# Kernel optimization log

Hardware: AMD Instinct MI355X
Metric: run time of the kernel (lower is better)

The kernel has to match this reference:

```python
import jax, jax.numpy as jnp
import numpy as np

B, N, D, H = 4, 4096, 128, 8
DH = D // H
EPS = 1e-6


def _layernorm(x, g, b):
    mu = jnp.mean(x, axis=-1, keepdims=True)
    var = jnp.var(x, axis=-1, keepdims=True)
    return (x - mu) * jax.lax.rsqrt(var + EPS) * g + b


def setup_inputs() -> dict:
    key = jax.random.key(0)
    ks = jax.random.split(key, 12)
    p = lambda k, shape: (jax.random.normal(k, shape, jnp.float32) * 0.02)
    x = jax.random.normal(ks[0], (B, N, D), jnp.float32)
    # scale fx so the sigmoid of the N-length contraction is not fully saturated
    fx = jax.random.normal(ks[1], (B, N, D), jnp.float32) / N
    return {
        "x": x,
        "fx": fx,
        "ln1_g": jnp.ones((D,), jnp.float32),
        "ln1_b": jnp.zeros((D,), jnp.float32),
        "wq": p(ks[2], (D, D)),
        "wk": p(ks[3], (D, D)),
        "wv": p(ks[4], (D, D)),
        "wo": p(ks[5], (D, D)),
        "bo": jnp.zeros((D,), jnp.float32),
        "ln2_g": jnp.ones((D,), jnp.float32),
        "ln2_b": jnp.zeros((D,), jnp.float32),
        "w1": p(ks[6], (D, D)),
        "b1": jnp.zeros((D,), jnp.float32),
        "w2": p(ks[7], (D, D)),
        "b2": jnp.zeros((D,), jnp.float32),
    }


def reference(x, fx, ln1_g, ln1_b, wq, wk, wv, wo, bo, ln2_g, ln2_b, w1, b1, w2, b2):
    b, n, d = x.shape
    h, dh = H, d // H
    # --- pre-norm linear self-attention ---
    xn = _layernorm(x, ln1_g, ln1_b)
    def heads(w):  # [b,n,d] @ w^T -> [b,h,n,dh]
        return jnp.einsum('bnd,ed->bne', xn, w).reshape(b, n, h, dh).transpose(0, 2, 1, 3)
    q = jax.nn.softmax(heads(wq), axis=-1)   # softmax over feature dim
    k = jax.nn.softmax(heads(wk), axis=2)    # softmax over sequence dim
    v = heads(wv)
    ctx = jnp.einsum('bhnd,bhne->bhde', k, v)         # [b,h,dh,dh]
    attn = jnp.einsum('bhnd,bhde->bhne', q, ctx)       # [b,h,n,dh]
    attn = attn.transpose(0, 2, 1, 3).reshape(b, n, d)
    attn = jnp.einsum('bnd,ed->bne', attn, wo) + bo
    x = x + attn                                       # residual (dropout=identity)
    # --- pre-norm MLP ---
    y = _layernorm(x, ln2_g, ln2_b)
    y = jax.nn.gelu(jnp.einsum('bnd,ed->bne', y, w1) + b1, approximate=False)
    y = jnp.einsum('bnd,ed->bne', y, w2) + b2
    x = x + y
    # --- quadratic update: sigmoid((x x^T) fx), as written in the module ---
    gram = jnp.einsum('bnd,bmd->bnm', x, x)            # [b,n,n] materialized, faithful
    fx = jax.nn.sigmoid(jnp.einsum('bnm,bmd->bnd', gram, fx))
    return (x, fx)
```

## Files before the change

kernel.cpp:

```cpp
#include <hip/hip_runtime.h>
#include <math.h>

#define BB 4
#define NN 4096
#define DD 128
#define MM (BB*NN)

typedef __attribute__((ext_vector_type(8))) short short8;
typedef __attribute__((ext_vector_type(4))) float f32x4;

__device__ inline short f2bf(float f) {
    unsigned u = __float_as_uint(f);
    u = (u + 0x7FFFu + ((u >> 16) & 1u)) >> 16;
    return (short)u;
}
__device__ inline float bf2f(short s) {
    return __uint_as_float(((unsigned)(unsigned short)s) << 16);
}
__device__ inline short8 pack_bf8(float4 a, float4 b) {
    short8 o;
    o[0] = f2bf(a.x); o[1] = f2bf(a.y); o[2] = f2bf(a.z); o[3] = f2bf(a.w);
    o[4] = f2bf(b.x); o[5] = f2bf(b.y); o[6] = f2bf(b.z); o[7] = f2bf(b.w);
    return o;
}
__device__ inline int swzoff(int row, int col) {
    return ((row * 128 + col) * 2) ^ ((row & 7) << 4);
}

__global__ __launch_bounds__(256) void wprep(const float* __restrict__ w0, const float* __restrict__ w1,
                                             const float* __restrict__ w2, const float* __restrict__ w3,
                                             const float* __restrict__ w4, short* __restrict__ wf) {
    int m = blockIdx.x >> 3;
    int j = (blockIdx.x & 7) * 256 + threadIdx.x;
    const float* W = (m == 0) ? w0 : (m == 1) ? w1 : (m == 2) ? w2 : (m == 3) ? w3 : w4;
    int nt = j >> 8, ks = (j >> 6) & 3, l = j & 63, r = l & 15, g = l >> 4;
    const float* src = W + (size_t)(nt * 16 + r) * DD + 32 * ks + 8 * g;
    float4 a = *(const float4*)src;
    float4 b = *(const float4*)(src + 4);
    ((short8*)(wf + (size_t)m * 16384))[j] = pack_bf8(a, b);
}

__global__ __launch_bounds__(256) void lnctx(const float* __restrict__ x,
                                             const float* __restrict__ lng,
                                             const float* __restrict__ lnb,
                                             const short* __restrict__ wf,
                                             float* __restrict__ partC,
                                             float* __restrict__ pcs) {
    __shared__ float ekL[32][132];
    __shared__ float vL[32][132];
    int t = threadIdx.x;
    int block_row = blockIdx.x * 32;
    int w = t >> 6, l = t & 63, r = l & 15, g = l >> 4;
    int rh = w >> 1, nt0 = (w & 1) << 2;
    int row0 = block_row + rh * 16;

    const float* ap = x + (size_t)(row0 + r) * DD + 8 * g;
    float4 av0[4], av1[4];
    #pragma unroll
    for (int ks = 0; ks < 4; ks++) {
        av0[ks] = *(const float4*)(ap + 32 * ks);
        av1[ks] = *(const float4*)(ap + 32 * ks + 4);
    }
    float s = 0.f, ss = 0.f;
    #pragma unroll
    for (int ks = 0; ks < 4; ks++) {
        float4 a = av0[ks], b = av1[ks];
        s  += a.x + a.y + a.z + a.w + b.x + b.y + b.z + b.w;
        ss += a.x*a.x + a.y*a.y + a.z*a.z + a.w*a.w + b.x*b.x + b.y*b.y + b.z*b.z + b.w*b.w;
    }
    s  += __shfl_xor(s, 16);  s  += __shfl_xor(s, 32);
    ss += __shfl_xor(ss, 16); ss += __shfl_xor(ss, 32);
    float mu = s * (1.0f / DD);
    float var = ss * (1.0f / DD) - mu * mu;
    float rs = rsqrtf(var + 1e-6f);

    short8 af[4];
    #pragma unroll
    for (int ks = 0; ks < 4; ks++) {
        float4 g0 = *(const float4*)(lng + 32 * ks + 8 * g);
        float4 g1 = *(const float4*)(lng + 32 * ks + 8 * g + 4);
        float4 b0 = *(const float4*)(lnb + 32 * ks + 8 * g);
        float4 b1 = *(const float4*)(lnb + 32 * ks + 8 * g + 4);
        float4 n0, n1;
        n0.x = (av0[ks].x - mu) * rs * g0.x + b0.x;
        n0.y = (av0[ks].y - mu) * rs * g0.y + b0.y;
        n0.z = (av0[ks].z - mu) * rs * g0.z + b0.z;
        n0.w = (av0[ks].w - mu) * rs * g0.w + b0.w;
        n1.x = (av1[ks].x - mu) * rs * g1.x + b1.x;
        n1.y = (av1[ks].y - mu) * rs * g1.y + b1.y;
        n1.z = (av1[ks].z - mu) * rs * g1.z + b1.z;
        n1.w = (av1[ks].w - mu) * rs * g1.w + b1.w;
        af[ks] = pack_bf8(n0, n1);
    }

    f32x4 acc[2][4];
    #pragma unroll
    for (int m = 0; m < 2; m++)
        #pragma unroll
        for (int n = 0; n < 4; n++) acc[m][n] = (f32x4){0.f, 0.f, 0.f, 0.f};
    const short8* wp8 = (const short8*)wf;
    #pragma unroll
    for (int ks = 0; ks < 4; ks++)
        #pragma unroll
        for (int m = 0; m < 2; m++)
            #pragma unroll
            for (int n = 0; n < 4; n++)
                acc[m][n] = __builtin_amdgcn_mfma_f32_16x16x32_bf16(
                    af[ks], wp8[(size_t)m * 2048 + ((nt0 + n) * 4 + ks) * 64 + l], acc[m][n], 0, 0, 0);

    #pragma unroll
    for (int n = 0; n < 4; n++) {
        int col = (nt0 + n) * 16 + r;
        #pragma unroll
        for (int j = 0; j < 4; j++) {
            int rowL = rh * 16 + 4 * g + j;
            ekL[rowL][col] = __expf(acc[0][n][j]);
            vL[rowL][col]  = acc[1][n][j];
        }
    }
    __syncthreads();

    int h = t >> 5, sub = t & 31, d = sub >> 1, e0 = (sub & 1) * 8;
    float cs = 0.f;
    float sc[8] = {0.f, 0.f, 0.f, 0.f, 0.f, 0.f, 0.f, 0.f};
    #pragma unroll 8
    for (int row = 0; row < 32; row++) {
        float ekv = ekL[row][h * 16 + d];
        float4 v0 = *(const float4*)&vL[row][h * 16 + e0];
        float4 v1 = *(const float4*)&vL[row][h * 16 + e0 + 4];
        sc[0] += ekv * v0.x; sc[1] += ekv * v0.y; sc[2] += ekv * v0.z; sc[3] += ekv * v0.w;
        sc[4] += ekv * v1.x; sc[5] += ekv * v1.y; sc[6] += ekv * v1.z; sc[7] += ekv * v1.w;
        cs += ekv;
    }
    float* cb = partC + (size_t)blockIdx.x * 2048 + h * 256 + d * 16 + e0;
    *(float4*)cb       = (float4){sc[0], sc[1], sc[2], sc[3]};
    *(float4*)(cb + 4) = (float4){sc[4], sc[5], sc[6], sc[7]};
    if ((sub & 1) == 0) pcs[(size_t)blockIdx.x * 128 + h * 16 + d] = cs;
}

__global__ __launch_bounds__(256) void ctxred(const float* __restrict__ part,
                                              float* __restrict__ ctxacc) {
    int k = blockIdx.x;
    int b = k >> 4, s0 = (k & 15) * 128;
    int t = threadIdx.x;
    int slot = s0 + (t & 127), half = t >> 7;
    float s = 0.f;
    #pragma unroll 8
    for (int c = half * 64; c < half * 64 + 64; c++)
        s += part[(size_t)((b << 7) + c) * 2048 + slot];
    __shared__ float red[128];
    if (half) red[t & 127] = s;
    __syncthreads();
    if (!half) ctxacc[(size_t)b * 2048 + slot] = s + red[t & 127];
}

__global__ __launch_bounds__(256) void build_mt_k(const float* __restrict__ ctxacc,
                                                  const float* __restrict__ pcs,
                                                  const float* __restrict__ wo,
                                                  short* __restrict__ mtfrag) {
    int b = blockIdx.x >> 3, nt = blockIdx.x & 7;
    int t = threadIdx.x;
    __shared__ float ctxL[2048];
    __shared__ float csL[128];
    __shared__ float woL[2048];
    #pragma unroll
    for (int i = 0; i < 8; i++) {
        int idx = i * 256 + t;
        ctxL[idx] = ctxacc[(size_t)b * 2048 + idx];
        woL[idx]  = wo[(size_t)(nt * 16) * DD + idx];
    }
    if (t < 128) {
        float s = 0.f;
        #pragma unroll 8
        for (int c = 0; c < 128; c++) s += pcs[(size_t)(b * 128 + c) * 128 + t];
        csL[t] = s;
    }
    __syncthreads();
    int ks = (t >> 6) & 3, l = t & 63, r = l & 15, g = l >> 4;
    short8 o;
    #pragma unroll
    for (int i2 = 0; i2 < 8; i2++) {
        int k = 32 * ks + 8 * g + i2;
        float inv = 1.0f / csL[k];
        const float* wrow = woL + r * DD + (k >> 4) * 16;
        float s = 0.f;
        #pragma unroll
        for (int eo = 0; eo < 16; eo++) s += ctxL[k * 16 + eo] * wrow[eo];
        o[i2] = f2bf(s * inv);
    }
    ((short8*)(mtfrag + (size_t)b * 16384))[nt * 256 + t] = o;
}

__global__ __launch_bounds__(256) void fused_mid(const float* __restrict__ x,
                                                 const float* __restrict__ ln1g,
                                                 const float* __restrict__ ln1b,
                                                 const short* __restrict__ wqf,
                                                 const short* __restrict__ mtf,
                                                 const float* __restrict__ bo,
                                                 const float* __restrict__ ln2g,
                                                 const float* __restrict__ ln2b,
                                                 const short* __restrict__ w1f,
                                                 const float* __restrict__ b1,
                                                 const short* __restrict__ w2f,
                                                 const float* __restrict__ b2,
                                                 float* __restrict__ xfinal,
                                                 short* __restrict__ xbf) {
    __shared__ __align__(16) char ex[32 * 128 * 2];
    __shared__ float ex2f[32][132];
    __shared__ float redS[4][16], redSS[4][16];
    int t = threadIdx.x;
    int block_row = blockIdx.x * 32;
    int w = t >> 6, l = t & 63, r = l & 15, g = l >> 4;
    int rh = w >> 1, nt0 = (w & 1) << 2;
    int row0 = block_row + rh * 16;
    int rrow = rh * 16 + r;

    const float* ap = x + (size_t)(row0 + r) * DD + 8 * g;
    float4 av0[4], av1[4];
    #pragma unroll
    for (int ks = 0; ks < 4; ks++) {
        av0[ks] = *(const float4*)(ap + 32 * ks);
        av1[ks] = *(const float4*)(ap + 32 * ks + 4);
    }
    if ((w & 1) == 0) {
        #pragma unroll
        for (int ks = 0; ks < 4; ks++) {
            *(float4*)&ex2f[rrow][32 * ks + 8 * g]     = av0[ks];
            *(float4*)&ex2f[rrow][32 * ks + 8 * g + 4] = av1[ks];
        }
    }
    float s = 0.f, ss = 0.f;
    #pragma unroll
    for (int ks = 0; ks < 4; ks++) {
        float4 a = av0[ks], b = av1[ks];
        s  += a.x + a.y + a.z + a.w + b.x + b.y + b.z + b.w;
        ss += a.x*a.x + a.y*a.y + a.z*a.z + a.w*a.w + b.x*b.x + b.y*b.y + b.z*b.z + b.w*b.w;
    }
    s  += __shfl_xor(s, 16);  s  += __shfl_xor(s, 32);
    ss += __shfl_xor(ss, 16); ss += __shfl_xor(ss, 32);
    float mu1 = s * (1.0f / DD);
    float var1 = ss * (1.0f / DD) - mu1 * mu1;
    float rs1 = rsqrtf(var1 + 1e-6f);
    short8 af[4];
    #pragma unroll
    for (int ks = 0; ks < 4; ks++) {
        float4 g0 = *(const float4*)(ln1g + 32 * ks + 8 * g);
        float4 g1 = *(const float4*)(ln1g + 32 * ks + 8 * g + 4);
        float4 b0 = *(const float4*)(ln1b + 32 * ks + 8 * g);
        float4 b1v = *(const float4*)(ln1b + 32 * ks + 8 * g + 4);
        float4 n0, n1;
        n0.x = (av0[ks].x - mu1) * rs1 * g0.x + b0.x;
        n0.y = (av0[ks].y - mu1) * rs1 * g0.y + b0.y;
        n0.z = (av0[ks].z - mu1) * rs1 * g0.z + b0.z;
        n0.w = (av0[ks].w - mu1) * rs1 * g0.w + b0.w;
        n1.x = (av1[ks].x - mu1) * rs1 * g1.x + b1v.x;
        n1.y = (av1[ks].y - mu1) * rs1 * g1.y + b1v.y;
        n1.z = (av1[ks].z - mu1) * rs1 * g1.z + b1v.z;
        n1.w = (av1[ks].w - mu1) * rs1 * g1.w + b1v.w;
        af[ks] = pack_bf8(n0, n1);
    }

    const short8* qp = (const short8*)wqf;
    f32x4 accq[4];
    #pragma unroll
    for (int n = 0; n < 4; n++) accq[n] = (f32x4){0.f, 0.f, 0.f, 0.f};
    #pragma unroll
    for (int ks = 0; ks < 4; ks++)
        #pragma unroll
        for (int n = 0; n < 4; n++)
            accq[n] = __builtin_amdgcn_mfma_f32_16x16x32_bf16(
                af[ks], qp[((nt0 + n) * 4 + ks) * 64 + l], accq[n], 0, 0, 0);
    #pragma unroll
    for (int n = 0; n < 4; n++) {
        int col = (nt0 + n) * 16 + r;
        #pragma unroll
        for (int j = 0; j < 4; j++) {
            float e = __expf(accq[n][j]);
            float sm = e;
            sm += __shfl_xor(sm, 1); sm += __shfl_xor(sm, 2);
            sm += __shfl_xor(sm, 4); sm += __shfl_xor(sm, 8);
            *(short*)(ex + swzoff(rh * 16 + 4 * g + j, col)) = f2bf(e / sm);
        }
    }
    __syncthreads();

    short8 qf[4];
    #pragma unroll
    for (int ks = 0; ks < 4; ks++)
        qf[ks] = *(const short8*)(ex + swzoff(rrow, 32 * ks + 8 * g));
    float xres[4][4];
    #pragma unroll
    for (int n = 0; n < 4; n++)
        #pragma unroll
        for (int j = 0; j < 4; j++)
            xres[n][j] = ex2f[rh * 16 + 4 * g + j][(nt0 + n) * 16 + r];

    const short8* mp = (const short8*)(mtf + (size_t)(block_row >> 12) * 16384);
    f32x4 acc[4];
    #pragma unroll
    for (int n = 0; n < 4; n++) acc[n] = (f32x4){0.f, 0.f, 0.f, 0.f};
    #pragma unroll
    for (int ks = 0; ks < 4; ks++)
        #pragma unroll
        for (int n = 0; n < 4; n++)
            acc[n] = __builtin_amdgcn_mfma_f32_16x16x32_bf16(
                qf[ks], mp[((nt0 + n) * 4 + ks) * 64 + l], acc[n], 0, 0, 0);

    float vv[4][4];
    #pragma unroll
    for (int n = 0; n < 4; n++) {
        int col = (nt0 + n) * 16 + r;
        float bv = bo[col];
        #pragma unroll
        for (int j = 0; j < 4; j++)
            vv[n][j] = acc[n][j] + bv + xres[n][j];
    }

    #pragma unroll
    for (int j = 0; j < 4; j++) {
        float s1  = vv[0][j] + vv[1][j] + vv[2][j] + vv[3][j];
        float s2 = vv[0][j]*vv[0][j] + vv[1][j]*vv[1][j] + vv[2][j]*vv[2][j] + vv[3][j]*vv[3][j];
        s1 += __shfl_xor(s1, 1); s1 += __shfl_xor(s1, 2); s1 += __shfl_xor(s1, 4); s1 += __shfl_xor(s1, 8);
        s2 += __shfl_xor(s2, 1); s2 += __shfl_xor(s2, 2); s2 += __shfl_xor(s2, 4); s2 += __shfl_xor(s2, 8);
        if (r == 0) { redS[w][4 * g + j] = s1; redSS[w][4 * g + j] = s2; }
    }
    __syncthreads();
    int base = w & 2;
    #pragma unroll
    for (int j = 0; j < 4; j++) {
        int rr = 4 * g + j;
        float S  = redS[base][rr]  + redS[base + 1][rr];
        float SS = redSS[base][rr] + redSS[base + 1][rr];
        float mu = S * (1.0f / DD);
        float var = SS * (1.0f / DD) - mu * mu;
        float rs = rsqrtf(var + 1e-6f);
        int rowL = rh * 16 + rr;
        #pragma unroll
        for (int n = 0; n < 4; n++) {
            int col = (nt0 + n) * 16 + r;
            float y = (vv[n][j] - mu) * rs * ln2g[col] + ln2b[col];
            *(short*)(ex + swzoff(rowL, col)) = f2bf(y);
        }
    }
    __syncthreads();
    short8 yf[4];
    #pragma unroll
    for (int ks = 0; ks < 4; ks++)
        yf[ks] = *(const short8*)(ex + swzoff(rrow, 32 * ks + 8 * g));
    __syncthreads();
    const short8* w1p = (const short8*)w1f;
    f32x4 acc2[4];
    #pragma unroll
    for (int n = 0; n < 4; n++) acc2[n] = (f32x4){0.f, 0.f, 0.f, 0.f};
    #pragma unroll
    for (int ks = 0; ks < 4; ks++)
        #pragma unroll
        for (int n = 0; n < 4; n++)
            acc2[n] = __builtin_amdgcn_mfma_f32_16x16x32_bf16(
                yf[ks], w1p[((nt0 + n) * 4 + ks) * 64 + l], acc2[n], 0, 0, 0);
    #pragma unroll
    for (int n = 0; n < 4; n++) {
        int col = (nt0 + n) * 16 + r;
        float bv = b1[col];
        #pragma unroll
        for (int j = 0; j < 4; j++) {
            float v = acc2[n][j] + bv;
            v = 0.5f * v * (1.0f + erff(v * 0.70710678118654752f));
            *(short*)(ex + swzoff(rh * 16 + 4 * g + j, col)) = f2bf(v);
        }
    }
    __syncthreads();
    short8 hf[4];
    #pragma unroll
    for (int ks = 0; ks < 4; ks++)
        hf[ks] = *(const short8*)(ex + swzoff(rrow, 32 * ks + 8 * g));
    const short8* w2p = (const short8*)w2f;
    f32x4 acc3[4];
    #pragma unroll
    for (int n = 0; n < 4; n++) acc3[n] = (f32x4){0.f, 0.f, 0.f, 0.f};
    #pragma unroll
    for (int ks = 0; ks < 4; ks++)
        #pragma unroll
        for (int n = 0; n < 4; n++)
            acc3[n] = __builtin_amdgcn_mfma_f32_16x16x32_bf16(
                hf[ks], w2p[((nt0 + n) * 4 + ks) * 64 + l], acc3[n], 0, 0, 0);
    #pragma unroll
    for (int n = 0; n < 4; n++) {
        int col = (nt0 + n) * 16 + r;
        float bv = b2[col];
        #pragma unroll
        for (int j = 0; j < 4; j++) {
            float v = acc3[n][j] + bv + vv[n][j];
            size_t row = (size_t)(row0 + 4 * g + j);
            xfinal[row * DD + col] = v;
            xbf[row * DD + col] = f2bf(v);
        }
    }
}

__global__ __launch_bounds__(512) void sbuild_p(const short* __restrict__ xf,
                                                const float* __restrict__ fx,
                                                short* __restrict__ part) {
    int b = blockIdx.x >> 6, chunk = blockIdx.x & 63;
    int t = threadIdx.x;
    __shared__ float xs[64 * 128], fs[64 * 128];
    const short* xb = xf + ((size_t)b * NN + chunk * 64) * DD;
    const float* fb = fx + ((size_t)b * NN + chunk * 64) * DD;
    const short8* xg = (const short8*)xb;
    float4* xs4 = (float4*)xs; float4* fs4 = (float4*)fs;
    const float4* fg = (const float4*)fb;
    #pragma unroll
    for (int i = 0; i < 2; i++) {
        int j = i * 512 + t;
        short8 s8 = xg[j];
        float4 a = {bf2f(s8[0]), bf2f(s8[1]), bf2f(s8[2]), bf2f(s8[3])};
        float4 c = {bf2f(s8[4]), bf2f(s8[5]), bf2f(s8[6]), bf2f(s8[7])};
        xs4[2 * j] = a; xs4[2 * j + 1] = c;
    }
    #pragma unroll
    for (int i = 0; i < 4; i++) {
        int j = i * 512 + t;
        fs4[j] = fg[j];
    }
    __syncthreads();
    int td = t & 15, te = t >> 4;
    float acc[8][4];
    #pragma unroll
    for (int a = 0; a < 8; a++)
        #pragma unroll
        for (int c = 0; c < 4; c++) acc[a][c] = 0.f;
    for (int r = 0; r < 64; r++) {
        float4 x0 = xs4[r * 32 + td * 2], x1 = xs4[r * 32 + td * 2 + 1];
        float4 f0 = fs4[r * 32 + te];
        float xv[8] = {x0.x, x0.y, x0.z, x0.w, x1.x, x1.y, x1.z, x1.w};
        float fv[4] = {f0.x, f0.y, f0.z, f0.w};
        #pragma unroll
        for (int a = 0; a < 8; a++)
            #pragma unroll
            for (int c = 0; c < 4; c++) acc[a][c] = fmaf(xv[a], fv[c], acc[a][c]);
    }
    short* pb = part + (size_t)blockIdx.x * 16384;
    #pragma unroll
    for (int ci = 0; ci < 4; ci++) {
        short8 o;
        #pragma unroll
        for (int a = 0; a < 8; a++) o[a] = f2bf(acc[a][ci]);
        *(short8*)(pb + (size_t)(te * 4 + ci) * 128 + td * 8) = o;
    }
}

__global__ __launch_bounds__(256) void sreduce2(const short* __restrict__ part,
                                                float* __restrict__ S_T) {
    int b = blockIdx.x >> 7, e = blockIdx.x & 127;
    int t = threadIdx.x;
    int d8 = (t & 15) * 8;
    int ch0 = t >> 4;
    float s[8] = {0.f, 0.f, 0.f, 0.f, 0.f, 0.f, 0.f, 0.f};
    #pragma unroll
    for (int cc = 0; cc < 4; cc++) {
        int ch = ch0 + cc * 16;
        short8 u = *(const short8*)(part + (size_t)(b * 64 + ch) * 16384 + e * 128 + d8);
        #pragma unroll
        for (int i = 0; i < 8; i++) s[i] += bf2f(u[i]);
    }
    #pragma unroll
    for (int i = 0; i < 8; i++) {
        s[i] += __shfl_xor(s[i], 16);
        s[i] += __shfl_xor(s[i], 32);
    }
    __shared__ float red[4][128];
    int w = t >> 6;
    if ((t & 63) < 16) {
        #pragma unroll
        for (int i = 0; i < 8; i++) red[w][d8 + i] = s[i];
    }
    __syncthreads();
    if (t < 128)
        S_T[((size_t)b * 128 + e) * 128 + t] = red[0][t] + red[1][t] + red[2][t] + red[3][t];
}

__global__ __launch_bounds__(256) void gemm_sig(const short* __restrict__ A,
                                                const float* __restrict__ S_T,
                                                float* __restrict__ Cf) {
    int t = threadIdx.x;
    int block_row = blockIdx.x * 32;
    int w = t >> 6, l = t & 63, r = l & 15, g = l >> 4;
    int row0 = block_row + ((w >> 1) << 4);
    int nt0 = (w & 1) << 2;
    const short8* ap = (const short8*)(A + (size_t)(row0 + r) * DD + 8 * g);
    short8 af[4];
    #pragma unroll
    for (int ks = 0; ks < 4; ks++) af[ks] = ap[ks * 4];
    const float* sp = S_T + (size_t)(block_row >> 12) * 16384;
    short8 bf[4][4];
// ... 23 lines not shown
        for (int j = 0; j < 4; j++) {
            float v = 1.0f / (1.0f + __expf(-acc[n][j]));
            Cf[(size_t)(row0 + 4 * g + j) * DD + col] = v;
        }
    }
}

extern "C" void kernel_launch(void* const* d_in, const int* in_sizes, int n_in,
                              void* d_out, int out_size, void* d_ws, size_t ws_size,
                              hipStream_t stream) {
    const float* x    = (const float*)d_in[0];
    const float* fx   = (const float*)d_in[1];
    const float* ln1g = (const float*)d_in[2];
    const float* ln1b = (const float*)d_in[3];
    const float* wq   = (const float*)d_in[4];
    const float* wk   = (const float*)d_in[5];
    const float* wv   = (const float*)d_in[6];
    const float* wo   = (const float*)d_in[7];
    const float* bo   = (const float*)d_in[8];
    const float* ln2g = (const float*)d_in[9];
    const float* ln2b = (const float*)d_in[10];
    const float* w1   = (const float*)d_in[11];
    const float* b1   = (const float*)d_in[12];
    const float* w2   = (const float*)d_in[13];
    const float* b2   = (const float*)d_in[14];

    float* out = (float*)d_out;
    float* xfinal = out;
    float* fxout  = out + (size_t)MM * DD;

    float* ws = (float*)d_ws;
    short* xbf    = (short*)ws;
    short* partSb = (short*)(ws + 1048576);
    short* wfW    = (short*)(ws + 3145728);
    float* partC  = ws + 3145728 + 40960;
    float* pcs    = partC + 1048576;
    float* ctxacc = pcs + 65536;
    float* S_T    = ctxacc + 8192;
    short* mtf    = (short*)(S_T + 65536);

    wprep<<<40, 256, 0, stream>>>(wq, wk, wv, w1, w2, wfW);
    lnctx<<<512, 256, 0, stream>>>(x, ln1g, ln1b, wfW + 16384, partC, pcs);
    ctxred<<<64, 256, 0, stream>>>(partC, ctxacc);
    build_mt_k<<<32, 256, 0, stream>>>(ctxacc, pcs, wo, mtf);
    fused_mid<<<512, 256, 0, stream>>>(x, ln1g, ln1b, wfW, mtf, bo, ln2g, ln2b,
                                       wfW + 3 * 16384, b1, wfW + 4 * 16384, b2,
                                       xfinal, xbf);
    sbuild_p<<<256, 512, 0, stream>>>(xbf, fx, partSb);
    sreduce2<<<512, 256, 0, stream>>>(partSb, S_T);
    gemm_sig<<<512, 256, 0, stream>>>(xbf, S_T, fxout);
}
```

Measured before the change: 73.06 us.

## Fuse x^T·fx partial-sum build into the mid MLP kernel

The separate sbuild_p kernel is removed. Its per-chunk x^T·fx partial products are now computed at the end of fused_mid from the fp32 x values already in registers, staged through a shared-memory arena. This drops one launch and the re-read of xbf and fx in a separate pass, and uses fp32 x instead of a bf16 round-trip. In exchange there are twice as many partial chunks (128 per batch of 32 rows), which doubles the partial-buffer writes and the sreduce2 reads. Shared-memory use per block also grows.

Measured after the change: 78.42 us. 1.07x slower.

```diff
diff --git a/kernel.cpp b/kernel.cpp
--- a/kernel.cpp
+++ b/kernel.cpp
@@ -191,23 +191,27 @@
     ((short8*)(mtfrag + (size_t)b * 16384))[nt * 256 + t] = o;
 }
 
-__global__ __launch_bounds__(256) void fused_mid(const float* __restrict__ x,
-                                                 const float* __restrict__ ln1g,
-                                                 const float* __restrict__ ln1b,
-                                                 const short* __restrict__ wqf,
-                                                 const short* __restrict__ mtf,
-                                                 const float* __restrict__ bo,
-                                                 const float* __restrict__ ln2g,
-                                                 const float* __restrict__ ln2b,
-                                                 const short* __restrict__ w1f,
-                                                 const float* __restrict__ b1,
-                                                 const short* __restrict__ w2f,
-                                                 const float* __restrict__ b2,
-                                                 float* __restrict__ xfinal,
-                                                 short* __restrict__ xbf) {
-    __shared__ __align__(16) char ex[32 * 128 * 2];
-    __shared__ float ex2f[32][132];
-    __shared__ float redS[4][16], redSS[4][16];
+__global__ __launch_bounds__(256) void fused_mid_s(const float* __restrict__ x,
+                                                   const float* __restrict__ fx,
+                                                   const float* __restrict__ ln1g,
+                                                   const float* __restrict__ ln1b,
+                                                   const short* __restrict__ wqf,
+                                                   const short* __restrict__ mtf,
+                                                   const float* __restrict__ bo,
+                                                   const float* __restrict__ ln2g,
+                                                   const float* __restrict__ ln2b,
+                                                   const short* __restrict__ w1f,
+                                                   const float* __restrict__ b1,
+                                                   const short* __restrict__ w2f,
+                                                   const float* __restrict__ b2,
+                                                   float* __restrict__ xfinal,
+                                                   short* __restrict__ xbf,
+                                                   short* __restrict__ partSb) {
+    __shared__ __align__(16) char arena[33792];
+    char* ex = arena;
+    float (*ex2f)[132] = (float(*)[132])(arena + 8192);
+    float (*redS)[16]  = (float(*)[16])(arena + 25088);
+    float (*redSS)[16] = (float(*)[16])(arena + 25344);
     int t = threadIdx.x;
     int block_row = blockIdx.x * 32;
     int w = t >> 6, l = t & 63, r = l & 15, g = l >> 4;
@@ -318,7 +322,7 @@
 
     #pragma unroll
     for (int j = 0; j < 4; j++) {
-        float s1  = vv[0][j] + vv[1][j] + vv[2][j] + vv[3][j];
+        float s1 = vv[0][j] + vv[1][j] + vv[2][j] + vv[3][j];
         float s2 = vv[0][j]*vv[0][j] + vv[1][j]*vv[1][j] + vv[2][j]*vv[2][j] + vv[3][j]*vv[3][j];
         s1 += __shfl_xor(s1, 1); s1 += __shfl_xor(s1, 2); s1 += __shfl_xor(s1, 4); s1 += __shfl_xor(s1, 8);
         s2 += __shfl_xor(s2, 1); s2 += __shfl_xor(s2, 2); s2 += __shfl_xor(s2, 4); s2 += __shfl_xor(s2, 8);
@@ -384,6 +388,7 @@
         for (int n = 0; n < 4; n++)
             acc3[n] = __builtin_amdgcn_mfma_f32_16x16x32_bf16(
                 hf[ks], w2p[((nt0 + n) * 4 + ks) * 64 + l], acc3[n], 0, 0, 0);
+    float xf_[4][4];
     #pragma unroll
     for (int n = 0; n < 4; n++) {
         int col = (nt0 + n) * 16 + r;
@@ -391,61 +396,58 @@
         #pragma unroll
         for (int j = 0; j < 4; j++) {
             float v = acc3[n][j] + bv + vv[n][j];
+            xf_[n][j] = v;
             size_t row = (size_t)(row0 + 4 * g + j);
             xfinal[row * DD + col] = v;
             xbf[row * DD + col] = f2bf(v);
         }
     }
-}
-
-__global__ __launch_bounds__(512) void sbuild_p(const short* __restrict__ xf,
-                                                const float* __restrict__ fx,
-                                                short* __restrict__ part) {
-    int b = blockIdx.x >> 6, chunk = blockIdx.x & 63;
-    int t = threadIdx.x;
-    __shared__ float xs[64 * 128], fs[64 * 128];
-    const short* xb = xf + ((size_t)b * NN + chunk * 64) * DD;
-    const float* fb = fx + ((size_t)b * NN + chunk * 64) * DD;
-    const short8* xg = (const short8*)xb;
-    float4* xs4 = (float4*)xs; float4* fs4 = (float4*)fs;
-    const float4* fg = (const float4*)fb;
-    #pragma unroll
-    for (int i = 0; i < 2; i++) {
-        int j = i * 512 + t;
-        short8 s8 = xg[j];
-        float4 a = {bf2f(s8[0]), bf2f(s8[1]), bf2f(s8[2]), bf2f(s8[3])};
-        float4 c = {bf2f(s8[4]), bf2f(s8[5]), bf2f(s8[6]), bf2f(s8[7])};
-        xs4[2 * j] = a; xs4[2 * j + 1] = c;
-    }
-    #pragma unroll
-    for (int i = 0; i < 4; i++) {
-        int j = i * 512 + t;
-        fs4[j] = fg[j];
-    }
-    __syncthreads();
-    int td = t & 15, te = t >> 4;
-    float acc[8][4];
-    #pragma unroll
-    for (int a = 0; a < 8; a++)
-        #pragma unroll
-        for (int c = 0; c < 4; c++) acc[a][c] = 0.f;
-    for (int r = 0; r < 64; r++) {
-        float4 x0 = xs4[r * 32 + td * 2], x1 = xs4[r * 32 + td * 2 + 1];
-        float4 f0 = fs4[r * 32 + te];
-        float xv[8] = {x0.x, x0.y, x0.z, x0.w, x1.x, x1.y, x1.z, x1.w};
-        float fv[4] = {f0.x, f0.y, f0.z, f0.w};
+
+    __syncthreads();
+    float* xsf = (float*)arena;
+    float* fsf = (float*)(arena + 16384);
+    {
+        const float4* fg = (const float4*)(fx + (size_t)block_row * DD);
+        float4* fsf4 = (float4*)fsf;
+        #pragma unroll
+        for (int i = 0; i < 4; i++) fsf4[i * 256 + t] = fg[i * 256 + t];
+        #pragma unroll
+        for (int n = 0; n < 4; n++) {
+            int col = (nt0 + n) * 16 + r;
+            #pragma unroll
+            for (int j = 0; j < 4; j++)
+                xsf[(rh * 16 + 4 * g + j) * 128 + col] = xf_[n][j];
+        }
+    }
+    __syncthreads();
+    {
+        int td = t >> 4, te = t & 15;
+        float accS[8][8];
         #pragma unroll
         for (int a = 0; a < 8; a++)
             #pragma unroll
-            for (int c = 0; c < 4; c++) acc[a][c] = fmaf(xv[a], fv[c], acc[a][c]);
-    }
-    short* pb = part + (size_t)blockIdx.x * 16384;
-    #pragma unroll
-    for (int ci = 0; ci < 4; ci++) {
-        short8 o;
-        #pragma unroll
-        for (int a = 0; a < 8; a++) o[a] = f2bf(acc[a][ci]);
-        *(short8*)(pb + (size_t)(te * 4 + ci) * 128 + td * 8) = o;
+            for (int c = 0; c < 8; c++) accS[a][c] = 0.f;
+        const float4* xs4 = (const float4*)xsf;
+        const float4* fs4 = (const float4*)fsf;
+        for (int row = 0; row < 32; row++) {
+            float4 x0 = xs4[row * 32 + td * 2], x1 = xs4[row * 32 + td * 2 + 1];
+            float4 f0 = fs4[row * 32 + te * 2], f1 = fs4[row * 32 + te * 2 + 1];
+            float xv[8] = {x0.x, x0.y, x0.z, x0.w, x1.x, x1.y, x1.z, x1.w};
+            float fv[8] = {f0.x, f0.y, f0.z, f0.w, f1.x, f1.y, f1.z, f1.w};
+            #pragma unroll
+            for (int a = 0; a < 8; a++)
+                #pragma unroll
+                for (int c = 0; c < 8; c++) accS[a][c] = fmaf(xv[a], fv[c], accS[a][c]);
+        }
+        short* pb = partSb + (size_t)blockIdx.x * 16384;
+        int d0 = td * 8, e0 = te * 8;
+        #pragma unroll
+        for (int ei = 0; ei < 8; ei++) {
+            short8 o;
+            #pragma unroll
+            for (int i = 0; i < 8; i++) o[i] = f2bf(accS[i][ei]);
+            *(short8*)(pb + (size_t)(e0 + ei) * DD + d0) = o;
+        }
     }
 }
 
@@ -457,9 +459,9 @@
     int ch0 = t >> 4;
     float s[8] = {0.f, 0.f, 0.f, 0.f, 0.f, 0.f, 0.f, 0.f};
     #pragma unroll
-    for (int cc = 0; cc < 4; cc++) {
+    for (int cc = 0; cc < 8; cc++) {
         int ch = ch0 + cc * 16;
-        short8 u = *(const short8*)(part + (size_t)(b * 64 + ch) * 16384 + e * 128 + d8);
+        short8 u = *(const short8*)(part + (size_t)(b * 128 + ch) * 16384 + e * 128 + d8);
         #pragma unroll
         for (int i = 0; i < 8; i++) s[i] += bf2f(u[i]);
     }
@@ -549,8 +551,8 @@
     float* ws = (float*)d_ws;
     short* xbf    = (short*)ws;
     short* partSb = (short*)(ws + 1048576);
-    short* wfW    = (short*)(ws + 3145728);
-    float* partC  = ws + 3145728 + 40960;
+    short* wfW    = (short*)(ws + 5242880);
+    float* partC  = ws + 5242880 + 40960;
     float* pcs    = partC + 1048576;
     float* ctxacc = pcs + 65536;
     float* S_T    = ctxacc + 8192;
@@ -560,10 +562,9 @@
     lnctx<<<512, 256, 0, stream>>>(x, ln1g, ln1b, wfW + 16384, partC, pcs);
     ctxred<<<64, 256, 0, stream>>>(partC, ctxacc);
     build_mt_k<<<32, 256, 0, stream>>>(ctxacc, pcs, wo, mtf);
-    fused_mid<<<512, 256, 0, stream>>>(x, ln1g, ln1b, wfW, mtf, bo, ln2g, ln2b,
-                                       wfW + 3 * 16384, b1, wfW + 4 * 16384, b2,
-                                       xfinal, xbf);
-    sbuild_p<<<256, 512, 0, stream>>>(xbf, fx, partSb);
+    fused_mid_s<<<512, 256, 0, stream>>>(x, fx, ln1g, ln1b, wfW, mtf, bo, ln2g, ln2b,
+                                         wfW + 3 * 16384, b1, wfW + 4 * 16384, b2,
+                                         xfinal, xbf, partSb);
     sreduce2<<<512, 256, 0, stream>>>(partSb, S_T);
     gemm_sig<<<512, 256, 0, stream>>>(xbf, S_T, fxout);
 }
```

## Split K dimension across wave pairs in fused_mid with LDS partial-sum reduction

Applied to the files above, without the earlier changes.

Doubles fused_mid's block to 512 threads, so each wave handles half of the K=128 contraction for every MFMA GEMM. The upper-half waves write their partial accumulators to LDS and the lower-half waves add them before the softmax, LayerNorm, GELU and output epilogues. The goal is more waves per block to hide latency, given only 512 blocks. In exchange it adds several extra __syncthreads and LDS round-trips per stage, and half the waves sit idle during the epilogues.

Measured after the change: 73.40 us. About the same (+0.5%).

```diff
diff --git a/kernel.cpp b/kernel.cpp
--- a/kernel.cpp
+++ b/kernel.cpp
@@ -191,7 +191,7 @@
     ((short8*)(mtfrag + (size_t)b * 16384))[nt * 256 + t] = o;
 }
 
-__global__ __launch_bounds__(256) void fused_mid(const float* __restrict__ x,
+__global__ __launch_bounds__(512) void fused_mid(const float* __restrict__ x,
                                                  const float* __restrict__ ln1g,
                                                  const float* __restrict__ ln1b,
                                                  const short* __restrict__ wqf,
@@ -205,59 +205,69 @@
                                                  const float* __restrict__ b2,
                                                  float* __restrict__ xfinal,
                                                  short* __restrict__ xbf) {
-    __shared__ __align__(16) char ex[32 * 128 * 2];
+    __shared__ __align__(16) char ex[8192];
     __shared__ float ex2f[32][132];
-    __shared__ float redS[4][16], redSS[4][16];
+    __shared__ f32x4 cbuf[16][64];
+    __shared__ float redA[8][16], redB[8][16];
+    __shared__ float redS[8][16], redSS[8][16];
     int t = threadIdx.x;
+    int w = t >> 6, l = t & 63, r = l & 15, g = l >> 4;
+    int rh = w >> 2, kh = (w >> 1) & 1, ch = w & 1;
+    int nt0 = ch * 4;
     int block_row = blockIdx.x * 32;
-    int w = t >> 6, l = t & 63, r = l & 15, g = l >> 4;
-    int rh = w >> 1, nt0 = (w & 1) << 2;
     int row0 = block_row + rh * 16;
     int rrow = rh * 16 + r;
-
-    const float* ap = x + (size_t)(row0 + r) * DD + 8 * g;
-    float4 av0[4], av1[4];
-    #pragma unroll
-    for (int ks = 0; ks < 4; ks++) {
-        av0[ks] = *(const float4*)(ap + 32 * ks);
-        av1[ks] = *(const float4*)(ap + 32 * ks + 4);
-    }
-    if ((w & 1) == 0) {
-        #pragma unroll
-        for (int ks = 0; ks < 4; ks++) {
-            *(float4*)&ex2f[rrow][32 * ks + 8 * g]     = av0[ks];
-            *(float4*)&ex2f[rrow][32 * ks + 8 * g + 4] = av1[ks];
+    int kbase = kh * 64;
+    int cslot = (rh * 2 + ch) * 4;
+
+    const float* ap = x + (size_t)(row0 + r) * DD + kbase + 8 * g;
+    float4 av0[2], av1[2];
+    #pragma unroll
+    for (int k2 = 0; k2 < 2; k2++) {
+        av0[k2] = *(const float4*)(ap + 32 * k2);
+        av1[k2] = *(const float4*)(ap + 32 * k2 + 4);
+    }
+    if (ch == 0) {
+        #pragma unroll
+        for (int k2 = 0; k2 < 2; k2++) {
+            *(float4*)&ex2f[rrow][kbase + 32 * k2 + 8 * g]     = av0[k2];
+            *(float4*)&ex2f[rrow][kbase + 32 * k2 + 8 * g + 4] = av1[k2];
         }
     }
     float s = 0.f, ss = 0.f;
     #pragma unroll
-    for (int ks = 0; ks < 4; ks++) {
-        float4 a = av0[ks], b = av1[ks];
+    for (int k2 = 0; k2 < 2; k2++) {
+        float4 a = av0[k2], b = av1[k2];
         s  += a.x + a.y + a.z + a.w + b.x + b.y + b.z + b.w;
         ss += a.x*a.x + a.y*a.y + a.z*a.z + a.w*a.w + b.x*b.x + b.y*b.y + b.z*b.z + b.w*b.w;
     }
     s  += __shfl_xor(s, 16);  s  += __shfl_xor(s, 32);
     ss += __shfl_xor(ss, 16); ss += __shfl_xor(ss, 32);
-    float mu1 = s * (1.0f / DD);
-    float var1 = ss * (1.0f / DD) - mu1 * mu1;
+    if (l < 16) { redA[w][l] = s; redB[w][l] = ss; }
+    __syncthreads();
+    float S1 = redA[rh * 4 + ch][r] + redA[rh * 4 + 2 + ch][r];
+    float S2 = redB[rh * 4 + ch][r] + redB[rh * 4 + 2 + ch][r];
+    float mu1 = S1 * (1.0f / DD);
+    float var1 = S2 * (1.0f / DD) - mu1 * mu1;
     float rs1 = rsqrtf(var1 + 1e-6f);
-    short8 af[4];
-    #pragma unroll
-    for (int ks = 0; ks < 4; ks++) {
-        float4 g0 = *(const float4*)(ln1g + 32 * ks + 8 * g);
-        float4 g1 = *(const float4*)(ln1g + 32 * ks + 8 * g + 4);
-        float4 b0 = *(const float4*)(ln1b + 32 * ks + 8 * g);
-        float4 b1v = *(const float4*)(ln1b + 32 * ks + 8 * g + 4);
+    short8 af[2];
+    #pragma unroll
+    for (int k2 = 0; k2 < 2; k2++) {
+        int co = kbase + 32 * k2 + 8 * g;
+        float4 g0 = *(const float4*)(ln1g + co);
+        float4 g1 = *(const float4*)(ln1g + co + 4);
+        float4 b0 = *(const float4*)(ln1b + co);
+        float4 b1v = *(const float4*)(ln1b + co + 4);
         float4 n0, n1;
-        n0.x = (av0[ks].x - mu1) * rs1 * g0.x + b0.x;
-        n0.y = (av0[ks].y - mu1) * rs1 * g0.y + b0.y;
-        n0.z = (av0[ks].z - mu1) * rs1 * g0.z + b0.z;
-        n0.w = (av0[ks].w - mu1) * rs1 * g0.w + b0.w;
-        n1.x = (av1[ks].x - mu1) * rs1 * g1.x + b1v.x;
-        n1.y = (av1[ks].y - mu1) * rs1 * g1.y + b1v.y;
-        n1.z = (av1[ks].z - mu1) * rs1 * g1.z + b1v.z;
-        n1.w = (av1[ks].w - mu1) * rs1 * g1.w + b1v.w;
-        af[ks] = pack_bf8(n0, n1);
+        n0.x = (av0[k2].x - mu1) * rs1 * g0.x + b0.x;
+        n0.y = (av0[k2].y - mu1) * rs1 * g0.y + b0.y;
+        n0.z = (av0[k2].z - mu1) * rs1 * g0.z + b0.z;
+        n0.w = (av0[k2].w - mu1) * rs1 * g0.w + b0.w;
+        n1.x = (av1[k2].x - mu1) * rs1 * g1.x + b1v.x;
+        n1.y = (av1[k2].y - mu1) * rs1 * g1.y + b1v.y;
+        n1.z = (av1[k2].z - mu1) * rs1 * g1.z + b1v.z;
+        n1.w = (av1[k2].w - mu1) * rs1 * g1.w + b1v.w;
+        af[k2] = pack_bf8(n0, n1);
     }
 
     const short8* qp = (const short8*)wqf;
@@ -265,135 +275,163 @@
     #pragma unroll
     for (int n = 0; n < 4; n++) accq[n] = (f32x4){0.f, 0.f, 0.f, 0.f};
     #pragma unroll
-    for (int ks = 0; ks < 4; ks++)
+    for (int k2 = 0; k2 < 2; k2++)
         #pragma unroll
         for (int n = 0; n < 4; n++)
             accq[n] = __builtin_amdgcn_mfma_f32_16x16x32_bf16(
-                af[ks], qp[((nt0 + n) * 4 + ks) * 64 + l], accq[n], 0, 0, 0);
-    #pragma unroll
-    for (int n = 0; n < 4; n++) {
-        int col = (nt0 + n) * 16 + r;
-        #pragma unroll
-        for (int j = 0; j < 4; j++) {
-            float e = __expf(accq[n][j]);
-            float sm = e;
-            sm += __shfl_xor(sm, 1); sm += __shfl_xor(sm, 2);
-            sm += __shfl_xor(sm, 4); sm += __shfl_xor(sm, 8);
-            *(short*)(ex + swzoff(rh * 16 + 4 * g + j, col)) = f2bf(e / sm);
-        }
-    }
-    __syncthreads();
-
-    short8 qf[4];
-    #pragma unroll
-    for (int ks = 0; ks < 4; ks++)
-        qf[ks] = *(const short8*)(ex + swzoff(rrow, 32 * ks + 8 * g));
-    float xres[4][4];
-    #pragma unroll
-    for (int n = 0; n < 4; n++)
-        #pragma unroll
-        for (int j = 0; j < 4; j++)
-            xres[n][j] = ex2f[rh * 16 + 4 * g + j][(nt0 + n) * 16 + r];
+                af[k2], qp[((nt0 + n) * 4 + kh * 2 + k2) * 64 + l], accq[n], 0, 0, 0);
+    if (kh == 1) {
+        #pragma unroll
+        for (int n = 0; n < 4; n++) cbuf[cslot + n][l] = accq[n];
+    }
+    __syncthreads();
+    if (kh == 0) {
+        #pragma unroll
+        for (int n = 0; n < 4; n++) {
+            accq[n] += cbuf[cslot + n][l];
+            int col = (nt0 + n) * 16 + r;
+            #pragma unroll
+            for (int j = 0; j < 4; j++) {
+                float e = __expf(accq[n][j]);
+                float sm = e;
+                sm += __shfl_xor(sm, 1); sm += __shfl_xor(sm, 2);
+                sm += __shfl_xor(sm, 4); sm += __shfl_xor(sm, 8);
+                *(short*)(ex + swzoff(rh * 16 + 4 * g + j, col)) = f2bf(e / sm);
+            }
+        }
+    }
+    __syncthreads();
+
+    short8 qf[2];
+    #pragma unroll
+    for (int k2 = 0; k2 < 2; k2++)
+        qf[k2] = *(const short8*)(ex + swzoff(rrow, kbase + 32 * k2 + 8 * g));
 
     const short8* mp = (const short8*)(mtf + (size_t)(block_row >> 12) * 16384);
     f32x4 acc[4];
     #pragma unroll
     for (int n = 0; n < 4; n++) acc[n] = (f32x4){0.f, 0.f, 0.f, 0.f};
     #pragma unroll
-    for (int ks = 0; ks < 4; ks++)
+    for (int k2 = 0; k2 < 2; k2++)
         #pragma unroll
         for (int n = 0; n < 4; n++)
             acc[n] = __builtin_amdgcn_mfma_f32_16x16x32_bf16(
-                qf[ks], mp[((nt0 + n) * 4 + ks) * 64 + l], acc[n], 0, 0, 0);
+                qf[k2], mp[((nt0 + n) * 4 + kh * 2 + k2) * 64 + l], acc[n], 0, 0, 0);
+    if (kh == 1) {
+        #pragma unroll
+        for (int n = 0; n < 4; n++) cbuf[cslot + n][l] = acc[n];
+    }
+    __syncthreads();
 
     float vv[4][4];
-    #pragma unroll
-    for (int n = 0; n < 4; n++) {
-        int col = (nt0 + n) * 16 + r;
-        float bv = bo[col];
-        #pragma unroll
-        for (int j = 0; j < 4; j++)
-            vv[n][j] = acc[n][j] + bv + xres[n][j];
-    }
-
-    #pragma unroll
-    for (int j = 0; j < 4; j++) {
-        float s1  = vv[0][j] + vv[1][j] + vv[2][j] + vv[3][j];
-        float s2 = vv[0][j]*vv[0][j] + vv[1][j]*vv[1][j] + vv[2][j]*vv[2][j] + vv[3][j]*vv[3][j];
-        s1 += __shfl_xor(s1, 1); s1 += __shfl_xor(s1, 2); s1 += __shfl_xor(s1, 4); s1 += __shfl_xor(s1, 8);
-        s2 += __shfl_xor(s2, 1); s2 += __shfl_xor(s2, 2); s2 += __shfl_xor(s2, 4); s2 += __shfl_xor(s2, 8);
-        if (r == 0) { redS[w][4 * g + j] = s1; redSS[w][4 * g + j] = s2; }
-    }
-    __syncthreads();
-    int base = w & 2;
-    #pragma unroll
-    for (int j = 0; j < 4; j++) {
-        int rr = 4 * g + j;
-        float S  = redS[base][rr]  + redS[base + 1][rr];
-        float SS = redSS[base][rr] + redSS[base + 1][rr];
-        float mu = S * (1.0f / DD);
-        float var = SS * (1.0f / DD) - mu * mu;
-        float rs = rsqrtf(var + 1e-6f);
-        int rowL = rh * 16 + rr;
+    if (kh == 0) {
         #pragma unroll
         for (int n = 0; n < 4; n++) {
+            acc[n] += cbuf[cslot + n][l];
             int col = (nt0 + n) * 16 + r;
-            float y = (vv[n][j] - mu) * rs * ln2g[col] + ln2b[col];
-            *(short*)(ex + swzoff(rowL, col)) = f2bf(y);
-        }
-    }
-    __syncthreads();
-    short8 yf[4];
-    #pragma unroll
-    for (int ks = 0; ks < 4; ks++)
-        yf[ks] = *(const short8*)(ex + swzoff(rrow, 32 * ks + 8 * g));
-    __syncthreads();
+            float bv = bo[col];
+            #pragma unroll
+            for (int j = 0; j < 4; j++)
+                vv[n][j] = acc[n][j] + bv + ex2f[rh * 16 + 4 * g + j][col];
+        }
+        #pragma unroll
+        for (int j = 0; j < 4; j++) {
+            float s1 = vv[0][j] + vv[1][j] + vv[2][j] + vv[3][j];
+            float s2 = vv[0][j]*vv[0][j] + vv[1][j]*vv[1][j] + vv[2][j]*vv[2][j] + vv[3][j]*vv[3][j];
+            s1 += __shfl_xor(s1, 1); s1 += __shfl_xor(s1, 2); s1 += __shfl_xor(s1, 4); s1 += __shfl_xor(s1, 8);
+            s2 += __shfl_xor(s2, 1); s2 += __shfl_xor(s2, 2); s2 += __shfl_xor(s2, 4); s2 += __shfl_xor(s2, 8);
+            if (r == 0) { redS[w][4 * g + j] = s1; redSS[w][4 * g + j] = s2; }
+        }
+    }
+    __syncthreads();
+    if (kh == 0) {
+        #pragma unroll
+        for (int j = 0; j < 4; j++) {
+            int rr = 4 * g + j;
+            float Sv  = redS[rh * 4 + 0][rr] + redS[rh * 4 + 1][rr];
+            float SSv = redSS[rh * 4 + 0][rr] + redSS[rh * 4 + 1][rr];
+            float mu = Sv * (1.0f / DD);
+            float var = SSv * (1.0f / DD) - mu * mu;
+            float rs = rsqrtf(var + 1e-6f);
+            #pragma unroll
+            for (int n = 0; n < 4; n++) {
+                int col = (nt0 + n) * 16 + r;
+                float y = (vv[n][j] - mu) * rs * ln2g[col] + ln2b[col];
+                *(short*)(ex + swzoff(rh * 16 + rr, col)) = f2bf(y);
+            }
+        }
+    }
+    __syncthreads();
+
+    short8 yf[2];
+    #pragma unroll
+    for (int k2 = 0; k2 < 2; k2++)
+        yf[k2] = *(const short8*)(ex + swzoff(rrow, kbase + 32 * k2 + 8 * g));
+
     const short8* w1p = (const short8*)w1f;
     f32x4 acc2[4];
     #pragma unroll
     for (int n = 0; n < 4; n++) acc2[n] = (f32x4){0.f, 0.f, 0.f, 0.f};
     #pragma unroll
-    for (int ks = 0; ks < 4; ks++)
+    for (int k2 = 0; k2 < 2; k2++)
         #pragma unroll
         for (int n = 0; n < 4; n++)
             acc2[n] = __builtin_amdgcn_mfma_f32_16x16x32_bf16(
-                yf[ks], w1p[((nt0 + n) * 4 + ks) * 64 + l], acc2[n], 0, 0, 0);
-    #pragma unroll
-    for (int n = 0; n < 4; n++) {
-        int col = (nt0 + n) * 16 + r;
-        float bv = b1[col];
-        #pragma unroll
-        for (int j = 0; j < 4; j++) {
-            float v = acc2[n][j] + bv;
-            v = 0.5f * v * (1.0f + erff(v * 0.70710678118654752f));
-            *(short*)(ex + swzoff(rh * 16 + 4 * g + j, col)) = f2bf(v);
-        }
-    }
-    __syncthreads();
-    short8 hf[4];
-    #pragma unroll
-    for (int ks = 0; ks < 4; ks++)
-        hf[ks] = *(const short8*)(ex + swzoff(rrow, 32 * ks + 8 * g));
+                yf[k2], w1p[((nt0 + n) * 4 + kh * 2 + k2) * 64 + l], acc2[n], 0, 0, 0);
+    if (kh == 1) {
+        #pragma unroll
+        for (int n = 0; n < 4; n++) cbuf[cslot + n][l] = acc2[n];
+    }
+    __syncthreads();
+    if (kh == 0) {
+        #pragma unroll
+        for (int n = 0; n < 4; n++) {
+            acc2[n] += cbuf[cslot + n][l];
+            int col = (nt0 + n) * 16 + r;
+            float bv = b1[col];
+            #pragma unroll
+            for (int j = 0; j < 4; j++) {
+                float v = acc2[n][j] + bv;
+                v = 0.5f * v * (1.0f + erff(v * 0.70710678118654752f));
+                *(short*)(ex + swzoff(rh * 16 + 4 * g + j, col)) = f2bf(v);
+            }
+        }
+    }
+    __syncthreads();
+
+    short8 hf[2];
+    #pragma unroll
+    for (int k2 = 0; k2 < 2; k2++)
+        hf[k2] = *(const short8*)(ex + swzoff(rrow, kbase + 32 * k2 + 8 * g));
+
     const short8* w2p = (const short8*)w2f;
     f32x4 acc3[4];
     #pragma unroll
     for (int n = 0; n < 4; n++) acc3[n] = (f32x4){0.f, 0.f, 0.f, 0.f};
     #pragma unroll
-    for (int ks = 0; ks < 4; ks++)
+    for (int k2 = 0; k2 < 2; k2++)
         #pragma unroll
         for (int n = 0; n < 4; n++)
             acc3[n] = __builtin_amdgcn_mfma_f32_16x16x32_bf16(
-                hf[ks], w2p[((nt0 + n) * 4 + ks) * 64 + l], acc3[n], 0, 0, 0);
-    #pragma unroll
-    for (int n = 0; n < 4; n++) {
-        int col = (nt0 + n) * 16 + r;
-        float bv = b2[col];
-        #pragma unroll
-        for (int j = 0; j < 4; j++) {
-            float v = acc3[n][j] + bv + vv[n][j];
-            size_t row = (size_t)(row0 + 4 * g + j);
-            xfinal[row * DD + col] = v;
-            xbf[row * DD + col] = f2bf(v);
+                hf[k2], w2p[((nt0 + n) * 4 + kh * 2 + k2) * 64 + l], acc3[n], 0, 0, 0);
+    if (kh == 1) {
+        #pragma unroll
+        for (int n = 0; n < 4; n++) cbuf[cslot + n][l] = acc3[n];
+    }
+    __syncthreads();
+    if (kh == 0) {
+        #pragma unroll
+        for (int n = 0; n < 4; n++) {
+            acc3[n] += cbuf[cslot + n][l];
+            int col = (nt0 + n) * 16 + r;
+            float bv = b2[col];
+            #pragma unroll
+            for (int j = 0; j < 4; j++) {
+                float v = acc3[n][j] + bv + vv[n][j];
+                size_t row = (size_t)(row0 + 4 * g + j);
+                xfinal[row * DD + col] = v;
+                xbf[row * DD + col] = f2bf(v);
+            }
         }
     }
 }
@@ -560,7 +598,7 @@
     lnctx<<<512, 256, 0, stream>>>(x, ln1g, ln1b, wfW + 16384, partC, pcs);
     ctxred<<<64, 256, 0, stream>>>(partC, ctxacc);
     build_mt_k<<<32, 256, 0, stream>>>(ctxacc, pcs, wo, mtf);
-    fused_mid<<<512, 256, 0, stream>>>(x, ln1g, ln1b, wfW, mtf, bo, ln2g, ln2b,
+    fused_mid<<<512, 512, 0, stream>>>(x, ln1g, ln1b, wfW, mtf, bo, ln2g, ln2b,
                                        wfW + 3 * 16384, b1, wfW + 4 * 16384, b2,
                                        xfinal, xbf);
     sbuild_p<<<256, 512, 0, stream>>>(xbf, fx, partSb);
```

## Fuse weight prep into context kernel, drop ctx reduction kernel, use tanh GELU

Applied to the files above, without the earlier changes.

Merges the weight-to-bf16 prep into the first attention-context kernel and doubles its rows per block (512 threads, 64 rows), halving the partial-context count. The separate context-reduction launch is removed and build_mt_k now sums the partials itself. K/V weights are converted inline from fp32 global memory rather than read from the prepped buffer. The erf GELU is replaced with a tanh-style sigmoid approximation, which changes numerics slightly, and build_mt_k's serial 64-partial reduction over only 32 blocks may become a new bottleneck.

New measurement: 80.22 us. +9.8%, slower.

```diff
diff --git a/kernel.cpp b/kernel.cpp
--- a/kernel.cpp
+++ b/kernel.cpp
@@ -26,33 +26,42 @@
 __device__ inline int swzoff(int row, int col) {
     return ((row * 128 + col) * 2) ^ ((row & 7) << 4);
 }
-
-__global__ __launch_bounds__(256) void wprep(const float* __restrict__ w0, const float* __restrict__ w1,
-                                             const float* __restrict__ w2, const float* __restrict__ w3,
-                                             const float* __restrict__ w4, short* __restrict__ wf) {
-    int m = blockIdx.x >> 3;
-    int j = (blockIdx.x & 7) * 256 + threadIdx.x;
-    const float* W = (m == 0) ? w0 : (m == 1) ? w1 : (m == 2) ? w2 : (m == 3) ? w3 : w4;
-    int nt = j >> 8, ks = (j >> 6) & 3, l = j & 63, r = l & 15, g = l >> 4;
-    const float* src = W + (size_t)(nt * 16 + r) * DD + 32 * ks + 8 * g;
-    float4 a = *(const float4*)src;
-    float4 b = *(const float4*)(src + 4);
-    ((short8*)(wf + (size_t)m * 16384))[j] = pack_bf8(a, b);
-}
-
-__global__ __launch_bounds__(256) void lnctx(const float* __restrict__ x,
-                                             const float* __restrict__ lng,
-                                             const float* __restrict__ lnb,
-                                             const short* __restrict__ wf,
-                                             float* __restrict__ partC,
-                                             float* __restrict__ pcs) {
-    __shared__ float ekL[32][132];
-    __shared__ float vL[32][132];
+__device__ inline float gelu_f(float v) {
+    float z = 1.5957691f * (v + 0.044715f * v * v * v);
+    return v / (1.0f + __expf(-z));
+}
+
+__global__ __launch_bounds__(512) void lnctx2(const float* __restrict__ x,
+                                              const float* __restrict__ lng,
+                                              const float* __restrict__ lnb,
+                                              const float* __restrict__ wq,
+                                              const float* __restrict__ wk,
+                                              const float* __restrict__ wv,
+                                              const float* __restrict__ w1,
+                                              const float* __restrict__ w2,
+                                              short* __restrict__ wfW,
+                                              float* __restrict__ partC,
+                                              float* __restrict__ pcs) {
+    __shared__ float ekL[64][132];
+    __shared__ float vL[64][132];
     int t = threadIdx.x;
-    int block_row = blockIdx.x * 32;
+    int bid = blockIdx.x;
+
+    if (bid < 40 && t < 256) {
+        int m = bid >> 3;
+        int j = (bid & 7) * 256 + t;
+        const float* W = (m == 0) ? wq : (m == 1) ? wk : (m == 2) ? wv : (m == 3) ? w1 : w2;
+        int nt = j >> 8, ks = (j >> 6) & 3, ll = j & 63, rr = ll & 15, gg = ll >> 4;
+        const float* src = W + (size_t)(nt * 16 + rr) * DD + 32 * ks + 8 * gg;
+        ((short8*)(wfW + (size_t)m * 16384))[j] = pack_bf8(*(const float4*)src, *(const float4*)(src + 4));
+    }
+
     int w = t >> 6, l = t & 63, r = l & 15, g = l >> 4;
-    int rh = w >> 1, nt0 = (w & 1) << 2;
-    int row0 = block_row + rh * 16;
+    int grp = w >> 2, wi = w & 3;
+    int rh = wi >> 1, nt0 = (wi & 1) << 2;
+    int block_row = bid * 64;
+    int row0 = block_row + grp * 32 + rh * 16;
+    int rowL0 = grp * 32 + rh * 16;
 
     const float* ap = x + (size_t)(row0 + r) * DD + 8 * g;
     float4 av0[4], av1[4];
@@ -98,63 +107,46 @@
     for (int m = 0; m < 2; m++)
         #pragma unroll
         for (int n = 0; n < 4; n++) acc[m][n] = (f32x4){0.f, 0.f, 0.f, 0.f};
-    const short8* wp8 = (const short8*)wf;
-    #pragma unroll
-    for (int ks = 0; ks < 4; ks++)
-        #pragma unroll
-        for (int m = 0; m < 2; m++)
+    #pragma unroll
+    for (int ks = 0; ks < 4; ks++)
+        #pragma unroll
+        for (int m = 0; m < 2; m++) {
+            const float* Wm = m ? wv : wk;
             #pragma unroll
-            for (int n = 0; n < 4; n++)
-                acc[m][n] = __builtin_amdgcn_mfma_f32_16x16x32_bf16(
-                    af[ks], wp8[(size_t)m * 2048 + ((nt0 + n) * 4 + ks) * 64 + l], acc[m][n], 0, 0, 0);
+            for (int n = 0; n < 4; n++) {
+                const float* wsrc = Wm + (size_t)((nt0 + n) * 16 + r) * DD + 32 * ks + 8 * g;
+                short8 bfr = pack_bf8(*(const float4*)wsrc, *(const float4*)(wsrc + 4));
+                acc[m][n] = __builtin_amdgcn_mfma_f32_16x16x32_bf16(af[ks], bfr, acc[m][n], 0, 0, 0);
+            }
+        }
 
     #pragma unroll
     for (int n = 0; n < 4; n++) {
         int col = (nt0 + n) * 16 + r;
         #pragma unroll
         for (int j = 0; j < 4; j++) {
-            int rowL = rh * 16 + 4 * g + j;
+            int rowL = rowL0 + 4 * g + j;
             ekL[rowL][col] = __expf(acc[0][n][j]);
             vL[rowL][col]  = acc[1][n][j];
         }
     }
     __syncthreads();
 
-    int h = t >> 5, sub = t & 31, d = sub >> 1, e0 = (sub & 1) * 8;
+    int h = w, d = l >> 2, e0 = (l & 3) * 4;
     float cs = 0.f;
-    float sc[8] = {0.f, 0.f, 0.f, 0.f, 0.f, 0.f, 0.f, 0.f};
+    float sc[4] = {0.f, 0.f, 0.f, 0.f};
     #pragma unroll 8
-    for (int row = 0; row < 32; row++) {
+    for (int row = 0; row < 64; row++) {
         float ekv = ekL[row][h * 16 + d];
         float4 v0 = *(const float4*)&vL[row][h * 16 + e0];
-        float4 v1 = *(const float4*)&vL[row][h * 16 + e0 + 4];
         sc[0] += ekv * v0.x; sc[1] += ekv * v0.y; sc[2] += ekv * v0.z; sc[3] += ekv * v0.w;
-        sc[4] += ekv * v1.x; sc[5] += ekv * v1.y; sc[6] += ekv * v1.z; sc[7] += ekv * v1.w;
         cs += ekv;
     }
-    float* cb = partC + (size_t)blockIdx.x * 2048 + h * 256 + d * 16 + e0;
-    *(float4*)cb       = (float4){sc[0], sc[1], sc[2], sc[3]};
-    *(float4*)(cb + 4) = (float4){sc[4], sc[5], sc[6], sc[7]};
-    if ((sub & 1) == 0) pcs[(size_t)blockIdx.x * 128 + h * 16 + d] = cs;
-}
-
-__global__ __launch_bounds__(256) void ctxred(const float* __restrict__ part,
-                                              float* __restrict__ ctxacc) {
-    int k = blockIdx.x;
-    int b = k >> 4, s0 = (k & 15) * 128;
-    int t = threadIdx.x;
-    int slot = s0 + (t & 127), half = t >> 7;
-    float s = 0.f;
-    #pragma unroll 8
-    for (int c = half * 64; c < half * 64 + 64; c++)
-        s += part[(size_t)((b << 7) + c) * 2048 + slot];
-    __shared__ float red[128];
-    if (half) red[t & 127] = s;
-    __syncthreads();
-    if (!half) ctxacc[(size_t)b * 2048 + slot] = s + red[t & 127];
-}
-
-__global__ __launch_bounds__(256) void build_mt_k(const float* __restrict__ ctxacc,
+    *(float4*)(partC + (size_t)bid * 2048 + h * 256 + d * 16 + e0) = (float4){sc[0], sc[1], sc[2], sc[3]};
+    if ((l & 3) == 0) pcs[(size_t)bid * 128 + h * 16 + d] = cs;
+}
+
+__global__ __launch_bounds__(256) void build_mt_k(const float* __restrict__ partC,
                                                   const float* __restrict__ pcs,
                                                   const float* __restrict__ wo,
                                                   short* __restrict__ mtfrag) {
@@ -163,16 +155,25 @@
     __shared__ float ctxL[2048];
     __shared__ float csL[128];
     __shared__ float woL[2048];
+    {
+        float s[8] = {0.f,0.f,0.f,0.f,0.f,0.f,0.f,0.f};
+        for (int c = 0; c < 64; c++) {
+            const float* pp = partC + (size_t)(b * 64 + c) * 2048 + t;
+            #pragma unroll
+            for (int i = 0; i < 8; i++) s[i] += pp[i * 256];
+        }
+        #pragma unroll
+        for (int i = 0; i < 8; i++) ctxL[i * 256 + t] = s[i];
+    }
     #pragma unroll
     for (int i = 0; i < 8; i++) {
         int idx = i * 256 + t;
-        ctxL[idx] = ctxacc[(size_t)b * 2048 + idx];
-        woL[idx]  = wo[(size_t)(nt * 16) * DD + idx];
+        woL[idx] = wo[(size_t)(nt * 16) * DD + idx];
     }
     if (t < 128) {
         float s = 0.f;
         #pragma unroll 8
-        for (int c = 0; c < 128; c++) s += pcs[(size_t)(b * 128 + c) * 128 + t];
+        for (int c = 0; c < 64; c++) s += pcs[(size_t)(b * 64 + c) * 128 + t];
         csL[t] = s;
     }
     __syncthreads();
@@ -318,7 +319,7 @@
 
     #pragma unroll
     for (int j = 0; j < 4; j++) {
-        float s1  = vv[0][j] + vv[1][j] + vv[2][j] + vv[3][j];
+        float s1 = vv[0][j] + vv[1][j] + vv[2][j] + vv[3][j];
         float s2 = vv[0][j]*vv[0][j] + vv[1][j]*vv[1][j] + vv[2][j]*vv[2][j] + vv[3][j]*vv[3][j];
         s1 += __shfl_xor(s1, 1); s1 += __shfl_xor(s1, 2); s1 += __shfl_xor(s1, 4); s1 += __shfl_xor(s1, 8);
         s2 += __shfl_xor(s2, 1); s2 += __shfl_xor(s2, 2); s2 += __shfl_xor(s2, 4); s2 += __shfl_xor(s2, 8);
@@ -364,8 +365,7 @@
         float bv = b1[col];
         #pragma unroll
         for (int j = 0; j < 4; j++) {
-            float v = acc2[n][j] + bv;
-            v = 0.5f * v * (1.0f + erff(v * 0.70710678118654752f));
+            float v = gelu_f(acc2[n][j] + bv);
             *(short*)(ex + swzoff(rh * 16 + 4 * g + j, col)) = f2bf(v);
         }
     }
@@ -551,15 +551,12 @@
     short* partSb = (short*)(ws + 1048576);
     short* wfW    = (short*)(ws + 3145728);
     float* partC  = ws + 3145728 + 40960;
-    float* pcs    = partC + 1048576;
-    float* ctxacc = pcs + 65536;
-    float* S_T    = ctxacc + 8192;
+    float* pcs    = partC + 524288;
+    float* S_T    = pcs + 32768;
     short* mtf    = (short*)(S_T + 65536);
 
-    wprep<<<40, 256, 0, stream>>>(wq, wk, wv, w1, w2, wfW);
-    lnctx<<<512, 256, 0, stream>>>(x, ln1g, ln1b, wfW + 16384, partC, pcs);
-    ctxred<<<64, 256, 0, stream>>>(partC, ctxacc);
-    build_mt_k<<<32, 256, 0, stream>>>(ctxacc, pcs, wo, mtf);
+    lnctx2<<<256, 512, 0, stream>>>(x, ln1g, ln1b, wq, wk, wv, w1, w2, wfW, partC, pcs);
+    build_mt_k<<<32, 256, 0, stream>>>(partC, pcs, wo, mtf);
     fused_mid<<<512, 256, 0, stream>>>(x, ln1g, ln1b, wfW, mtf, bo, ln2g, ln2b,
                                        wfW + 3 * 16384, b1, wfW + 4 * 16384, b2,
                                        xfinal, xbf);
```
